# Kernel tuning notes

Measured on AMD Instinct MI355X. Metric: run time of the kernel, lower is better.

## Reference

```python
import jax, jax.numpy as jnp
import numpy as np

B = 64        # graphs per batch
N = 128       # nodes per graph (equal-sized graphs -> static shapes)
EMB = 16      # gm_val feature dim
OUT = 64      # output edge feature dim
E_REAL = 65536
FILL_VALUE = 0.0


def setup_inputs() -> dict:
    key = jax.random.key(0)
    k1, k2, k3, k4, k5 = jax.random.split(key, 5)

    num_nodes = B * N
    batch = jnp.asarray(np.arange(num_nodes) // N, dtype=jnp.int64)

    # gm_index: all within-graph node pairs, row-major per graph (matches full_edge_index order)
    loc = np.arange(N)
    src_l = np.repeat(loc, N)            # [N*N]
    dst_l = np.tile(loc, N)              # [N*N]
    off = (np.arange(B) * N)[:, None]    # [B,1]
    gm_src = (off + src_l[None, :]).reshape(-1)
    gm_dst = (off + dst_l[None, :]).reshape(-1)
    gm_index = jnp.asarray(np.stack([gm_src, gm_dst]), dtype=jnp.int64)  # [2, B*N*N]

    gm_val = jax.random.normal(k1, (B * N * N, EMB), dtype=jnp.float32)

    # real edges: random within each graph, E_REAL/B edges per graph
    eg = E_REAL // B
    src_loc = jax.random.randint(k2, (B, eg), 0, N)
    dst_loc = jax.random.randint(k3, (B, eg), 0, N)
    goff = (jnp.arange(B) * N)[:, None]
    edge_index = jnp.stack([(src_loc + goff).reshape(-1),
                            (dst_loc + goff).reshape(-1)]).astype(jnp.int64)

    edge_attr = jax.random.normal(k4, (E_REAL, OUT), dtype=jnp.float32)

    # fc weight, xavier-uniform-like init, shape [out_dim, emb_dim] (torch Linear layout)
    bound = float(np.sqrt(6.0 / (EMB + OUT)))
    W = jax.random.uniform(k5, (OUT, EMB), minval=-bound, maxval=bound, dtype=jnp.float32)

    return {"batch": batch, "edge_index": edge_index, "edge_attr": edge_attr,
            "gm_index": gm_index, "gm_val": gm_val, "W": W}


def _flat_id(idx):
    # map global (src, dst) within-graph pair to flat position in coalesced
    # (graph-major, row-major) full edge ordering. Graphs are equal-sized.
    src, dst = idx[0], idx[1]
    g = src // N
    return g * (N * N) + (src - g * N) * N + (dst - g * N)


def reference(batch, edge_index, edge_attr, gm_index, gm_val, W):
    total = B * N * N
    # FC(gm_val): [E_gm, EMB] @ [EMB, OUT]
    gm_proj = gm_val @ W.T

    # coalesce(cat([edge_index, gm_index, full_index]), op='add') over equal-sized
    # graphs yields exactly the sorted full pair set; values are scatter-added.
    out_val = jnp.full((total, OUT), FILL_VALUE, dtype=edge_attr.dtype)  # padding for all pairs
    out_val = out_val.at[_flat_id(edge_index)].add(edge_attr)
    out_val = out_val.at[_flat_id(gm_index)].add(gm_proj)

    # coalesced (sorted, deduped) index = full pair set in graph/row-major order
    flat = jnp.arange(total)
    g = flat // (N * N)
    rem = flat % (N * N)
    out_idx = jnp.stack([g * N + rem // N, g * N + rem % N]).astype(edge_index.dtype)
    return out_idx, out_val
```

## Files before the change

kernel.cpp:

```cpp
#include <hip/hip_runtime.h>

#define BGRAPH 64
#define NNODE  128
#define EMB    16
#define OUTF   64
#define EREAL  65536
#define TOTAL  (BGRAPH * NNODE * NNODE)

typedef float floatx4 __attribute__((ext_vector_type(4)));

#define SLOT_CAP 8

__global__ __launch_bounds__(256) void init_kernel(
    uint4* __restrict__ cnt4,
    float* __restrict__ out_idx)
{
    int t  = blockIdx.x * 256 + threadIdx.x;
    cnt4[t] = make_uint4(0u, 0u, 0u, 0u);

    int p0  = t * 4;
    int g   = p0 >> 14;
    int rem = p0 & 16383;
    float sv = (float)(g * NNODE + (rem >> 7));
    float dbase = (float)(g * NNODE + (rem & 127));
    floatx4 s = {sv, sv, sv, sv};
    floatx4 d = {dbase, dbase + 1.f, dbase + 2.f, dbase + 3.f};
    *(floatx4*)(out_idx + p0)          = s;
    *(floatx4*)(out_idx + TOTAL + p0)  = d;
}

__global__ __launch_bounds__(256) void bin_kernel(
    const int* __restrict__ edge_index,
    unsigned* __restrict__ cnt,
    unsigned* __restrict__ slots)
{
    int e = blockIdx.x * 256 + threadIdx.x;
    int src = edge_index[e];
    int dst = edge_index[EREAL + e];
    int fid = src * NNODE + (dst & (NNODE - 1));
    unsigned pos = atomicAdd(&cnt[fid], 1u);
    if (pos < SLOT_CAP)
        slots[(size_t)fid * SLOT_CAP + pos] = (unsigned)e;
}

#define CHUNK 256
#define GEMM_BLOCKS (TOTAL / CHUNK)

template <bool FUSED>
__global__ __launch_bounds__(256) void gemm_lds_kernel(
    const float* __restrict__ gm_val,
    const float* __restrict__ W,
    const unsigned* __restrict__ cnt,
    const unsigned* __restrict__ slots,
    const float* __restrict__ edge_attr,
    float* __restrict__ out_val)
{
    __shared__ float lds[CHUNK * EMB];
    const int tid  = threadIdx.x;
    const int oq   = tid & 15;
    const int grp  = tid >> 4;
    const int base = blockIdx.x * CHUNK;

    const floatx4* src = (const floatx4*)(gm_val + (size_t)base * EMB);
    floatx4 s0 = src[tid];
    floatx4 s1 = src[tid + 256];
    floatx4 s2 = src[tid + 512];
    floatx4 s3 = src[tid + 768];

    unsigned cv = 0;
    if (FUSED) cv = cnt[base + grp + 16 * oq];

    float w[4][16];
    const floatx4* W4 = (const floatx4*)W + oq * 16;
    #pragma unroll
    for (int j = 0; j < 4; ++j) {
        #pragma unroll
        for (int q = 0; q < 4; ++q) {
            floatx4 t = W4[j * 4 + q];
            w[j][q * 4 + 0] = t.x;
            w[j][q * 4 + 1] = t.y;
            w[j][q * 4 + 2] = t.z;
            w[j][q * 4 + 3] = t.w;
        }
    }

    floatx4* ldsf4 = (floatx4*)lds;
    ldsf4[tid]       = s0;
    ldsf4[tid + 256] = s1;
    ldsf4[tid + 512] = s2;
    ldsf4[tid + 768] = s3;
    __syncthreads();

    for (int s = 0; s < 16; ++s) {
        const int r = base + grp + 16 * s;
        const floatx4* rowp = ldsf4 + (size_t)(grp + 16 * s) * 4;
        floatx4 a = rowp[0], b = rowp[1], c = rowp[2], d = rowp[3];
        float v[16] = {a.x,a.y,a.z,a.w, b.x,b.y,b.z,b.w,
                       c.x,c.y,c.z,c.w, d.x,d.y,d.z,d.w};

        float t0 = 0.f, t1 = 0.f, t2 = 0.f, t3 = 0.f;
        #pragma unroll
        for (int k = 0; k < EMB; ++k) {
            t0 += v[k] * w[0][k];
            t1 += v[k] * w[1][k];
            t2 += v[k] * w[2][k];
            t3 += v[k] * w[3][k];
        }
        floatx4 o = {t0, t1, t2, t3};

        if (FUSED) {
            unsigned cR = __shfl(cv, s, 16);
            if (cR) {
                unsigned nE = cR < SLOT_CAP ? cR : SLOT_CAP;
                for (unsigned i = 0; i < nE; ++i) {
                    unsigned e = slots[(size_t)r * SLOT_CAP + i];
                    o += *(const floatx4*)(edge_attr + (size_t)e * OUTF + oq * 4);
                }
            }
        }
        __builtin_nontemporal_store(o, (floatx4*)(out_val + (size_t)r * OUTF + oq * 4));
    }
}

#define SCATTER_BLOCKS ((EREAL * OUTF) / 256)
#define IDX_BLOCKS (TOTAL / 256)

__global__ __launch_bounds__(256) void scatter_idx_kernel(
    const int* __restrict__ edge_index,
    const float* __restrict__ edge_attr,
    float* __restrict__ out_val,
    float* __restrict__ out_idx)
{
    int bid = blockIdx.x;
    if (bid < SCATTER_BLOCKS) {
        int idx = bid * 256 + threadIdx.x;
        int e = idx >> 6;
        int o = idx & 63;
        int src = edge_index[e];
        int dst = edge_index[EREAL + e];
        int fid = src * NNODE + (dst & (NNODE - 1));
        float a = __builtin_nontemporal_load(edge_attr + (size_t)e * OUTF + o);
        atomicAdd(out_val + (size_t)fid * OUTF + o, a);
    } else {
        int p = (bid - SCATTER_BLOCKS) * 256 + threadIdx.x;
        int g   = p >> 14;
        int rem = p & 16383;
        out_idx[p]         = (float)(g * NNODE + (rem >> 7));
        out_idx[TOTAL + p] = (float)(g * NNODE + (rem & 127));
    }
}

extern "C" void kernel_launch(void* const* d_in, const int* in_sizes, int n_in,
                              void* d_out, int out_size, void* d_ws, size_t ws_size,
                              hipStream_t stream)
{
    const int*   edge_index = (const int*)d_in[1];
    const float* edge_attr  = (const float*)d_in[2];
    const float* gm_val     = (const float*)d_in[4];
    const float* W          = (const float*)d_in[5];

    float* out      = (float*)d_out;
    float* out_idx  = out;
    float* out_val  = out + (size_t)2 * TOTAL;

    const size_t ws_need = (size_t)TOTAL * 4 + (size_t)TOTAL * SLOT_CAP * 4;

    if (ws_size >= ws_need) {
        unsigned* cnt   = (unsigned*)d_ws;
        unsigned* slots = cnt + TOTAL;
        init_kernel<<<TOTAL / 4 / 256, 256, 0, stream>>>((uint4*)cnt, out_idx);
        bin_kernel<<<EREAL / 256, 256, 0, stream>>>(edge_index, cnt, slots);
        gemm_lds_kernel<true><<<GEMM_BLOCKS, 256, 0, stream>>>(
            gm_val, W, cnt, slots, edge_attr, out_val);
    } else {
        gemm_lds_kernel<false><<<GEMM_BLOCKS, 256, 0, stream>>>(
            gm_val, W, nullptr, nullptr, nullptr, out_val);
        scatter_idx_kernel<<<SCATTER_BLOCKS + IDX_BLOCKS, 256, 0, stream>>>(
            edge_index, edge_attr, out_val, out_idx);
    }
}
```

Measured before the change: 375.9 us.

## Make GEMM blocks persistent over chunks with double-buffered LDS prefetch

The GEMM+scatter kernel now launches a fixed 1024 blocks, and each block walks 4 consecutive 256-row chunks. The next chunk's gm_val rows and counts are prefetched into registers while the current chunk computes, using two LDS buffers. This amortises the W register load per block and hides global load latency. It also replaces the nontemporal stores and loads with ordinary ones, which may change cache behaviour for the large streaming output.

Measured after the change: 392.1 us. +4.3%, slower.

```diff
diff --git a/kernel.cpp b/kernel.cpp
--- a/kernel.cpp
+++ b/kernel.cpp
@@ -44,7 +44,8 @@
 }
 
 #define CHUNK 256
-#define GEMM_BLOCKS (TOTAL / CHUNK)
+#define NBLOCKS 1024
+#define NCHUNK (TOTAL / (CHUNK * NBLOCKS))
 
 template <bool FUSED>
 __global__ __launch_bounds__(256) void gemm_lds_kernel(
@@ -55,20 +56,19 @@
     const float* __restrict__ edge_attr,
     float* __restrict__ out_val)
 {
-    __shared__ float lds[CHUNK * EMB];
+    __shared__ floatx4 lds[2][CHUNK * 4];
     const int tid  = threadIdx.x;
     const int oq   = tid & 15;
     const int grp  = tid >> 4;
-    const int base = blockIdx.x * CHUNK;
+    const int chunk0 = blockIdx.x * NCHUNK;
 
-    const floatx4* src = (const floatx4*)(gm_val + (size_t)base * EMB);
+    const floatx4* src = (const floatx4*)gm_val + (size_t)chunk0 * CHUNK * 4;
     floatx4 s0 = src[tid];
     floatx4 s1 = src[tid + 256];
     floatx4 s2 = src[tid + 512];
     floatx4 s3 = src[tid + 768];
-
     unsigned cv = 0;
-    if (FUSED) cv = cnt[base + grp + 16 * oq];
+    if (FUSED) cv = cnt[chunk0 * CHUNK + grp + 16 * oq];
 
     float w[4][16];
     const floatx4* W4 = (const floatx4*)W + oq * 16;
@@ -84,41 +84,58 @@
         }
     }
 
-    floatx4* ldsf4 = (floatx4*)lds;
-    ldsf4[tid]       = s0;
-    ldsf4[tid + 256] = s1;
-    ldsf4[tid + 512] = s2;
-    ldsf4[tid + 768] = s3;
-    __syncthreads();
+    #pragma unroll
+    for (int j = 0; j < NCHUNK; ++j) {
+        floatx4* buf = lds[j & 1];
+        buf[tid]       = s0;
+        buf[tid + 256] = s1;
+        buf[tid + 512] = s2;
+        buf[tid + 768] = s3;
+        __syncthreads();
 
-    for (int s = 0; s < 16; ++s) {
-        const int r = base + grp + 16 * s;
-        const floatx4* rowp = ldsf4 + (size_t)(grp + 16 * s) * 4;
-        floatx4 a = rowp[0], b = rowp[1], c = rowp[2], d = rowp[3];
-        float v[16] = {a.x,a.y,a.z,a.w, b.x,b.y,b.z,b.w,
-                       c.x,c.y,c.z,c.w, d.x,d.y,d.z,d.w};
+        const int base = (chunk0 + j) * CHUNK;
+        const unsigned cv_cur = cv;
 
-        float t0 = 0.f, t1 = 0.f, t2 = 0.f, t3 = 0.f;
-        #pragma unroll
-        for (int k = 0; k < EMB; ++k) {
-            t0 += v[k] * w[0][k];
-            t1 += v[k] * w[1][k];
-            t2 += v[k] * w[2][k];
-            t3 += v[k] * w[3][k];
+        if (j + 1 < NCHUNK) {
+            const floatx4* nsrc = (const floatx4*)gm_val
+                                  + (size_t)(chunk0 + j + 1) * CHUNK * 4;
+            s0 = nsrc[tid];
+            s1 = nsrc[tid + 256];
+            s2 = nsrc[tid + 512];
+            s3 = nsrc[tid + 768];
+            if (FUSED) cv = cnt[(chunk0 + j + 1) * CHUNK + grp + 16 * oq];
         }
-        floatx4 o = {t0, t1, t2, t3};
 
-        if (FUSED) {
-            unsigned cR = __shfl(cv, s, 16);
-            if (cR) {
-                unsigned nE = cR < SLOT_CAP ? cR : SLOT_CAP;
-                for (unsigned i = 0; i < nE; ++i) {
-                    unsigned e = slots[(size_t)r * SLOT_CAP + i];
-                    o += *(const floatx4*)(edge_attr + (size_t)e * OUTF + oq * 4);
+        #pragma unroll 2
+        for (int s = 0; s < 16; ++s) {
+            const int r = base + grp + 16 * s;
+            const floatx4* rowp = buf + (grp + 16 * s) * 4;
+            floatx4 a = rowp[0], b = rowp[1], c = rowp[2], d = rowp[3];
+            float v[16] = {a.x,a.y,a.z,a.w, b.x,b.y,b.z,b.w,
+                           c.x,c.y,c.z,c.w, d.x,d.y,d.z,d.w};
+
+            float t0 = 0.f, t1 = 0.f, t2 = 0.f, t3 = 0.f;
+            #pragma unroll
+            for (int k = 0; k < EMB; ++k) {
+                t0 += v[k] * w[0][k];
+                t1 += v[k] * w[1][k];
+                t2 += v[k] * w[2][k];
+                t3 += v[k] * w[3][k];
+            }
+            floatx4 o = {t0, t1, t2, t3};
+
+            if (FUSED) {
+                unsigned cR = __shfl(cv_cur, s, 16);
+                if (cR) {
+                    unsigned nE = cR < SLOT_CAP ? cR : SLOT_CAP;
+                    for (unsigned i = 0; i < nE; ++i) {
+                        unsigned e = slots[(size_t)r * SLOT_CAP + i];
+                        o += *(const floatx4*)(edge_attr + (size_t)e * OUTF + oq * 4);
+                    }
                 }
             }
+            *(floatx4*)(out_val + (size_t)r * OUTF + oq * 4) = o;
         }
-        __builtin_nontemporal_store(o, (floatx4*)(out_val + (size_t)r * OUTF + oq * 4));
     }
 }
 
@@ -139,8 +156,7 @@
         int src = edge_index[e];
         int dst = edge_index[EREAL + e];
         int fid = src * NNODE + (dst & (NNODE - 1));
-        float a = __builtin_nontemporal_load(edge_attr + (size_t)e * OUTF + o);
-        atomicAdd(out_val + (size_t)fid * OUTF + o, a);
+        atomicAdd(out_val + (size_t)fid * OUTF + o, edge_attr[(size_t)e * OUTF + o]);
     } else {
         int p = (bid - SCATTER_BLOCKS) * 256 + threadIdx.x;
         int g   = p >> 14;
@@ -170,10 +186,10 @@
         unsigned* slots = cnt + TOTAL;
         init_kernel<<<TOTAL / 4 / 256, 256, 0, stream>>>((uint4*)cnt, out_idx);
         bin_kernel<<<EREAL / 256, 256, 0, stream>>>(edge_index, cnt, slots);
-        gemm_lds_kernel<true><<<GEMM_BLOCKS, 256, 0, stream>>>(
+        gemm_lds_kernel<true><<<NBLOCKS, 256, 0, stream>>>(
             gm_val, W, cnt, slots, edge_attr, out_val);
     } else {
-        gemm_lds_kernel<false><<<GEMM_BLOCKS, 256, 0, stream>>>(
+        gemm_lds_kernel<false><<<NBLOCKS, 256, 0, stream>>>(
             gm_val, W, nullptr, nullptr, nullptr, out_val);
         scatter_idx_kernel<<<SCATTER_BLOCKS + IDX_BLOCKS, 256, 0, stream>>>(
             edge_index, edge_attr, out_val, out_idx);
```
